# Kernel optimization log

Measured on AMD Instinct MI355X. Metric: run time of the kernel, lower is better.

## Reference

```python
import jax, jax.numpy as jnp
import numpy as np

V, BLOCK, D, H, L = 32000, 2048, 768, 12, 4
B, T = 2, 2048
HD = D // H
FF = 4 * D


def setup_inputs() -> dict:
    key = jax.random.key(0)
    ks = jax.random.split(key, 20)
    s = 0.02
    inp = {
        "idx": jax.random.randint(ks[0], (B, T), 0, V),
        "tok_emb": jax.random.normal(ks[1], (V, D), jnp.float32) * s,
        "pos_emb": jax.random.normal(ks[2], (BLOCK, D), jnp.float32) * s,
        # per-layer stacked params (leading dim L); linear weights stored [in, out]
        "ln1_w": jnp.ones((L, D), jnp.float32),
        "ln1_b": jnp.zeros((L, D), jnp.float32),
        "Wqkv": jax.random.normal(ks[3], (L, D, 3 * D), jnp.float32) * s,
        "bqkv": jnp.zeros((L, 3 * D), jnp.float32),
        "Wproj": jax.random.normal(ks[4], (L, D, D), jnp.float32) * s,
        "bproj": jnp.zeros((L, D), jnp.float32),
        "ln2_w": jnp.ones((L, D), jnp.float32),
        "ln2_b": jnp.zeros((L, D), jnp.float32),
        "Wfc": jax.random.normal(ks[5], (L, D, FF), jnp.float32) * s,
        "bfc": jnp.zeros((L, FF), jnp.float32),
        "Wfc2": jax.random.normal(ks[6], (L, FF, D), jnp.float32) * s,
        "bfc2": jnp.zeros((L, D), jnp.float32),
        "lnf_w": jnp.ones((D,), jnp.float32),
        "lnf_b": jnp.zeros((D,), jnp.float32),
    }
    return inp


def _layernorm(x, w, b, eps=1e-5):
    mu = jnp.mean(x, axis=-1, keepdims=True)
    var = jnp.var(x, axis=-1, keepdims=True)
    return (x - mu) * jax.lax.rsqrt(var + eps) * w + b


def _attn(x, Wqkv, bqkv, Wproj, bproj):
    b, t, c = x.shape
    qkv = x @ Wqkv + bqkv  # [B,T,3D]
    q, k, v = jnp.split(qkv, 3, axis=-1)
    q = q.reshape(b, t, H, HD)
    k = k.reshape(b, t, H, HD)
    v = v.reshape(b, t, H, HD)
    scale = 1.0 / np.sqrt(HD)
    att = jnp.einsum("bthd,bshd->bhts", q, k) * scale  # [B,H,T,T]
    causal = jnp.tril(jnp.ones((t, t), bool))
    att = jnp.where(causal[None, None], att, -jnp.inf)
    att = jax.nn.softmax(att, axis=-1)
    out = jnp.einsum("bhts,bshd->bthd", att, v).reshape(b, t, c)
    return out @ Wproj + bproj


def reference(idx, tok_emb, pos_emb, ln1_w, ln1_b, Wqkv, bqkv, Wproj, bproj,
              ln2_w, ln2_b, Wfc, bfc, Wfc2, bfc2, lnf_w, lnf_b):
    t = idx.shape[1]
    x = tok_emb[idx] + pos_emb[:t][None]  # [B,T,D]
    for l in range(L):
        h = _layernorm(x, ln1_w[l], ln1_b[l])
        x = x + _attn(h, Wqkv[l], bqkv[l], Wproj[l], bproj[l])
        h = _layernorm(x, ln2_w[l], ln2_b[l])
        h = jax.nn.gelu(h @ Wfc[l] + bfc[l], approximate=False) @ Wfc2[l] + bfc2[l]
        x = x + h
    x = _layernorm(x, lnf_w, lnf_b)
    return x @ tok_emb.T  # tied head, [B,T,V]
```

## Files before the change

kernel.cpp:

```cpp
#include <hip/hip_runtime.h>
#include <math.h>

#define VOCAB  32000
#define DMODEL 768
#define NHEAD  12
#define NLAYER 4
#define BATCH  2
#define SEQ    2048
#define HEADD  64
#define FFDIM  3072
#define MROWS  (BATCH*SEQ)

typedef __attribute__((ext_vector_type(8))) short bf16x8;
typedef __attribute__((ext_vector_type(4))) float f32x4;

__device__ __forceinline__ unsigned short f2bf(float f) {
    union { float f; unsigned u; } v; v.f = f;
    unsigned r = v.u + 0x7fffu + ((v.u >> 16) & 1u);
    return (unsigned short)(r >> 16);
}

__device__ __forceinline__ void async_lds16(const unsigned short* g, unsigned short* l) {
    __builtin_amdgcn_global_load_lds(
        (const __attribute__((address_space(1))) unsigned int*)(const void*)g,
        (__attribute__((address_space(3))) unsigned int*)(void*)l, 16, 0, 0);
}

__global__ void cvt_bf16_x4(const float* __restrict__ in, unsigned short* __restrict__ out, int n4) {
    int i = blockIdx.x * blockDim.x + threadIdx.x;
    if (i >= n4) return;
    float4 v = ((const float4*)in)[i];
    uint2 o;
    o.x = (unsigned)f2bf(v.x) | ((unsigned)f2bf(v.y) << 16);
    o.y = (unsigned)f2bf(v.z) | ((unsigned)f2bf(v.w) << 16);
    ((uint2*)out)[i] = o;
}

__global__ void transpose_cvt(const float* __restrict__ W, unsigned short* __restrict__ Wt,
                              int Kdim, int Ndim) {
    __shared__ float tile[32][33];
    int l  = blockIdx.z;
    int k0 = blockIdx.x * 32;
    int n0 = blockIdx.y * 32;
    const float* Wl = W + (size_t)l * Kdim * Ndim;
    unsigned short* Wtl = Wt + (size_t)l * Kdim * Ndim;
    int c = threadIdx.x & 31, r = threadIdx.x >> 5;
#pragma unroll
    for (int i = 0; i < 4; i++)
        tile[r + i * 8][c] = Wl[(size_t)(k0 + r + i * 8) * Ndim + n0 + c];
    __syncthreads();
#pragma unroll
    for (int i = 0; i < 4; i++)
        Wtl[(size_t)(n0 + r + i * 8) * Kdim + k0 + c] = f2bf(tile[c][r + i * 8]);
}

__global__ void embed_kernel(const int* __restrict__ idx, const float* __restrict__ tok,
                             const float* __restrict__ pos, float* __restrict__ x) {
    int row = blockIdx.x;
    int t = row & (SEQ - 1);
    int tr = idx[row];
    const float4* ts = (const float4*)(tok + (size_t)tr * DMODEL);
    const float4* ps = (const float4*)(pos + (size_t)t * DMODEL);
    float4* xs = (float4*)(x + (size_t)row * DMODEL);
    int i = threadIdx.x;
    float4 a = ts[i], b = ps[i];
    xs[i] = make_float4(a.x + b.x, a.y + b.y, a.z + b.z, a.w + b.w);
}

__global__ void layernorm_kernel(const float* __restrict__ x, const float* __restrict__ w,
                                 const float* __restrict__ b, unsigned short* __restrict__ out) {
    int row = blockIdx.x;
    const float* xr = x + (size_t)row * DMODEL;
    int t = threadIdx.x;
    float v0 = xr[t], v1 = xr[t + 256], v2 = xr[t + 512];
    float s = v0 + v1 + v2;
    float ss = v0 * v0 + v1 * v1 + v2 * v2;
#pragma unroll
    for (int off = 32; off >= 1; off >>= 1) {
        s  += __shfl_xor(s, off);
        ss += __shfl_xor(ss, off);
    }
    __shared__ float red[8];
    int wave = t >> 6, lane = t & 63;
    if (lane == 0) { red[wave] = s; red[wave + 4] = ss; }
    __syncthreads();
    s  = red[0] + red[1] + red[2] + red[3];
    ss = red[4] + red[5] + red[6] + red[7];
    float mu = s * (1.0f / DMODEL);
    float var = ss * (1.0f / DMODEL) - mu * mu;
    float rs = rsqrtf(var + 1e-5f);
    unsigned short* orow = out + (size_t)row * DMODEL;
    orow[t]       = f2bf((v0 - mu) * rs * w[t]       + b[t]);
    orow[t + 256] = f2bf((v1 - mu) * rs * w[t + 256] + b[t + 256]);
    orow[t + 512] = f2bf((v2 - mu) * rs * w[t + 512] + b[t + 512]);
}

template <bool GELU_, bool RESID_, bool OUTBF16_, bool BIAS_>
__global__ __launch_bounds__(256) void gemm_kernel(
    const unsigned short* __restrict__ A,
    const unsigned short* __restrict__ Bw,
    const float* __restrict__ bias,
    const float* resid,
    float* Cf, unsigned short* Cb,
    int Ndim, int Kdim) {
    const int bm = blockIdx.x * 128;
    const int bn = blockIdx.y * 128;
    __shared__ unsigned short As[128][32];
    __shared__ unsigned short Bs[128][32];
    int tid = threadIdx.x;
    int wave = tid >> 6, lane = tid & 63;
    int wm = (wave >> 1) * 64, wn = (wave & 1) * 64;
    int quad = lane >> 4, ln = lane & 15;
    int srow = lane >> 2;
    int scol = (lane & 3) * 8;
    f32x4 acc[4][4] = {};

    for (int k0 = 0; k0 < Kdim; k0 += 32) {
        __syncthreads();
#pragma unroll
        for (int i = 0; i < 2; i++) {
            int ch = (wave << 1) | i;
            async_lds16(A  + (size_t)(bm + ch * 16 + srow) * Kdim + k0 + scol, &As[ch * 16][0]);
            async_lds16(Bw + (size_t)(bn + ch * 16 + srow) * Kdim + k0 + scol, &Bs[ch * 16][0]);
        }
        __syncthreads();
        bf16x8 af[4], bfr[4];
#pragma unroll
        for (int tm = 0; tm < 4; tm++) af[tm]  = *(const bf16x8*)(&As[wm + tm * 16 + ln][quad * 8]);
#pragma unroll
        for (int tn = 0; tn < 4; tn++) bfr[tn] = *(const bf16x8*)(&Bs[wn + tn * 16 + ln][quad * 8]);
#pragma unroll
        for (int tm = 0; tm < 4; tm++)
#pragma unroll
            for (int tn = 0; tn < 4; tn++)
                acc[tm][tn] = __builtin_amdgcn_mfma_f32_16x16x32_bf16(af[tm], bfr[tn], acc[tm][tn], 0, 0, 0);
    }

#pragma unroll
    for (int tm = 0; tm < 4; tm++)
#pragma unroll
        for (int tn = 0; tn < 4; tn++)
#pragma unroll
            for (int r = 0; r < 4; r++) {
                int row = bm + wm + tm * 16 + quad * 4 + r;
                int col = bn + wn + tn * 16 + ln;
                float c = acc[tm][tn][r];
                if (BIAS_) c += bias[col];
                if (GELU_) c = 0.5f * c * (1.0f + erff(c * 0.70710678118654752f));
                if (RESID_) c += resid[(size_t)row * Ndim + col];
                if (OUTBF16_) Cb[(size_t)row * Ndim + col] = f2bf(c);
                else          Cf[(size_t)row * Ndim + col] = c;
            }
}

__global__ __launch_bounds__(256) void attn_kernel(const unsigned short* __restrict__ qkv,
                                                   unsigned short* __restrict__ out) {
    int qtile = blockIdx.x;
    int bh = blockIdx.y;
    int b = bh / NHEAD, h = bh % NHEAD;
    int q0 = qtile * 128;
    const unsigned short* base = qkv + (size_t)b * SEQ * (3 * DMODEL);

    __shared__ unsigned short Qs[128][72];
    __shared__ unsigned short Ks[64][72];
    __shared__ unsigned short Vs[64][72];
    __shared__ unsigned short Ps[128][72];

    int tid = threadIdx.x, wave = tid >> 6, lane = tid & 63;
    int quad = lane >> 4, ln = lane & 15;

    for (int c = tid; c < 1024; c += 256) {
        int r = c >> 3, col = (c & 7) * 8;
        *(bf16x8*)(&Qs[r][col]) =
            *(const bf16x8*)(base + (size_t)(q0 + r) * (3 * DMODEL) + h * HEADD + col);
    }
    __syncthreads();

    bf16x8 qf[2][2];
#pragma unroll
    for (int tm = 0; tm < 2; tm++)
#pragma unroll
        for (int ks = 0; ks < 2; ks++)
            qf[tm][ks] = *(const bf16x8*)(&Qs[wave * 32 + tm * 16 + ln][ks * 32 + quad * 8]);

    f32x4 o[2][4] = {};
    float mst[8], lst[8];
#pragma unroll
    for (int i = 0; i < 8; i++) { mst[i] = -3.0e38f; lst[i] = 0.0f; }

    const float scale = 0.125f;
    int nkt = qtile * 2 + 2;

    for (int kt = 0; kt < nkt; kt++) {
        __syncthreads();
        for (int c = tid; c < 512; c += 256) {
            int r = c >> 3, col = (c & 7) * 8;
            *(bf16x8*)(&Ks[r][col]) =
                *(const bf16x8*)(base + (size_t)(kt * 64 + r) * (3 * DMODEL) + DMODEL + h * HEADD + col);
            union { bf16x8 v; unsigned short u[8]; } vv;
            vv.v = *(const bf16x8*)(base + (size_t)(kt * 64 + r) * (3 * DMODEL) + 2 * DMODEL + h * HEADD + col);
#pragma unroll
            for (int j = 0; j < 8; j++) Vs[col + j][r] = vv.u[j];
        }
        __syncthreads();

        f32x4 s[2][4];
#pragma unroll
        for (int tm = 0; tm < 2; tm++)
#pragma unroll
            for (int tn = 0; tn < 4; tn++) s[tm][tn] = (f32x4){0.f, 0.f, 0.f, 0.f};
        bf16x8 kf[4][2];
#pragma unroll
        for (int tn = 0; tn < 4; tn++)
#pragma unroll
            for (int ks = 0; ks < 2; ks++)
                kf[tn][ks] = *(const bf16x8*)(&Ks[tn * 16 + ln][ks * 32 + quad * 8]);
#pragma unroll
        for (int tm = 0; tm < 2; tm++)
#pragma unroll
            for (int tn = 0; tn < 4; tn++)
#pragma unroll
                for (int ks = 0; ks < 2; ks++)
                    s[tm][tn] = __builtin_amdgcn_mfma_f32_16x16x32_bf16(qf[tm][ks], kf[tn][ks], s[tm][tn], 0, 0, 0);

#pragma unroll
        for (int tm = 0; tm < 2; tm++)
#pragma unroll
            for (int tn = 0; tn < 4; tn++)
#pragma unroll
                for (int r = 0; r < 4; r++) {
                    int qi = q0 + wave * 32 + tm * 16 + quad * 4 + r;
                    int kj = kt * 64 + tn * 16 + ln;
                    float sv = s[tm][tn][r] * scale;
                    s[tm][tn][r] = (kj > qi) ? -3.0e38f : sv;
                }

#pragma unroll
        for (int tm = 0; tm < 2; tm++)
#pragma unroll
            for (int r = 0; r < 4; r++) {
                float mx = fmaxf(fmaxf(s[tm][0][r], s[tm][1][r]), fmaxf(s[tm][2][r], s[tm][3][r]));
#pragma unroll
                for (int msk = 1; msk <= 8; msk <<= 1) mx = fmaxf(mx, __shfl_xor(mx, msk));
                int ri = tm * 4 + r;
                float mnew = fmaxf(mst[ri], mx);
                float alpha = __expf(mst[ri] - mnew);
                mst[ri] = mnew;
                float psum = 0.f;
#pragma unroll
                for (int tn = 0; tn < 4; tn++) {
                    float p = __expf(s[tm][tn][r] - mnew);
                    s[tm][tn][r] = p;
                    psum += p;
                }
#pragma unroll
                for (int msk = 1; msk <= 8; msk <<= 1) psum += __shfl_xor(psum, msk);
                lst[ri] = lst[ri] * alpha + psum;
#pragma unroll
                for (int nd = 0; nd < 4; nd++) o[tm][nd][r] *= alpha;
            }

#pragma unroll
        for (int tm = 0; tm < 2; tm++)
#pragma unroll
            for (int tn = 0; tn < 4; tn++)
#pragma unroll
                for (int r = 0; r < 4; r++)
                    Ps[wave * 32 + tm * 16 + quad * 4 + r][tn * 16 + ln] = f2bf(s[tm][tn][r]);

        bf16x8 pf[2][2], vf[4][2];
#pragma unroll
        for (int tm = 0; tm < 2; tm++)
#pragma unroll
            for (int ks = 0; ks < 2; ks++)
                pf[tm][ks] = *(const bf16x8*)(&Ps[wave * 32 + tm * 16 + ln][ks * 32 + quad * 8]);
#pragma unroll
        for (int nd = 0; nd < 4; nd++)
#pragma unroll
            for (int ks = 0; ks < 2; ks++)
                vf[nd][ks] = *(const bf16x8*)(&Vs[nd * 16 + ln][ks * 32 + quad * 8]);
#pragma unroll
        for (int tm = 0; tm < 2; tm++)
#pragma unroll
            for (int nd = 0; nd < 4; nd++)
#pragma unroll
                for (int ks = 0; ks < 2; ks++)
                    o[tm][nd] = __builtin_amdgcn_mfma_f32_16x16x32_bf16(pf[tm][ks], vf[nd][ks], o[tm][nd], 0, 0, 0);
    }

#pragma unroll
    for (int tm = 0; tm < 2; tm++)
#pragma unroll
        for (int r = 0; r < 4; r++) {
            float inv = 1.0f / lst[tm * 4 + r];
            int trow = q0 + wave * 32 + tm * 16 + quad * 4 + r;
#pragma unroll
            for (int nd = 0; nd < 4; nd++) {
                int col = h * HEADD + nd * 16 + ln;
                out[(size_t)(b * SEQ + trow) * DMODEL + col] = f2bf(o[tm][nd][r] * inv);
            }
        }
}

extern "C" void kernel_launch(void* const* d_in, const int* in_sizes, int n_in,
                              void* d_out, int out_size, void* d_ws, size_t ws_size,
                              hipStream_t stream) {
    const int*   idx   = (const int*)  d_in[0];
    const float* tok   = (const float*)d_in[1];
    const float* pos   = (const float*)d_in[2];
    const float* ln1w  = (const float*)d_in[3];
    const float* ln1b  = (const float*)d_in[4];
    const float* Wqkv  = (const float*)d_in[5];
    const float* bqkv  = (const float*)d_in[6];
    const float* Wproj = (const float*)d_in[7];
    const float* bproj = (const float*)d_in[8];
    const float* ln2w  = (const float*)d_in[9];
    const float* ln2b  = (const float*)d_in[10];
    const float* Wfc   = (const float*)d_in[11];
    const float* bfc   = (const float*)d_in[12];
    const float* Wfc2  = (const float*)d_in[13];
    const float* bfc2  = (const float*)d_in[14];
    const float* lnfw  = (const float*)d_in[15];
    const float* lnfb  = (const float*)d_in[16];

    char* ob = (char*)d_out;
    unsigned short* qkvb   = (unsigned short*)(ob + 0);
    float*          x      = (float*)(ob + 18874368);
    unsigned short* ffact  = (unsigned short*)(ob + 31457280);
    unsigned short* attnb  = (unsigned short*)(ob + 56623104);
    unsigned short* WqkvT  = (unsigned short*)(ob + 62914560);
    unsigned short* WprojT = (unsigned short*)(ob + 77070336);
    unsigned short* WfcT   = (unsigned short*)(ob + 81788928);
    unsigned short* Wfc2T  = (unsigned short*)(ob + 100663296);
    unsigned short* tokT   = (unsigned short*)d_ws;
    unsigned short* lnout  = (unsigned short*)((char*)d_ws + 49152000);

    cvt_bf16_x4<<<24000, 256, 0, stream>>>(tok, tokT, VOCAB * DMODEL / 4);
    transpose_cvt<<<dim3(24, 72, NLAYER), 256, 0, stream>>>(Wqkv,  WqkvT,  DMODEL, 3 * DMODEL);
    transpose_cvt<<<dim3(24, 24, NLAYER), 256, 0, stream>>>(Wproj, WprojT, DMODEL, DMODEL);
    transpose_cvt<<<dim3(24, 96, NLAYER), 256, 0, stream>>>(Wfc,   WfcT,   DMODEL, FFDIM);
    transpose_cvt<<<dim3(96, 24, NLAYER), 256, 0, stream>>>(Wfc2,  Wfc2T,  FFDIM,  DMODEL);

    embed_kernel<<<MROWS, 192, 0, stream>>>(idx, tok, pos, x);

    for (int l = 0; l < NLAYER; l++) {
        layernorm_kernel<<<MROWS, 256, 0, stream>>>(x, ln1w + l * DMODEL, ln1b + l * DMODEL, lnout);
        gemm_kernel<false, false, true, true><<<dim3(32, 18), 256, 0, stream>>>(
            lnout, WqkvT + (size_t)l * 3 * DMODEL * DMODEL, bqkv + l * 3 * DMODEL,
            nullptr, nullptr, qkvb, 3 * DMODEL, DMODEL);
        attn_kernel<<<dim3(16, BATCH * NHEAD), 256, 0, stream>>>(qkvb, attnb);
        gemm_kernel<false, true, false, true><<<dim3(32, 6), 256, 0, stream>>>(
            attnb, WprojT + (size_t)l * DMODEL * DMODEL, bproj + l * DMODEL,
            x, x, nullptr, DMODEL, DMODEL);
        layernorm_kernel<<<MROWS, 256, 0, stream>>>(x, ln2w + l * DMODEL, ln2b + l * DMODEL, lnout);
        gemm_kernel<true, false, true, true><<<dim3(32, 24), 256, 0, stream>>>(
            lnout, WfcT + (size_t)l * FFDIM * DMODEL, bfc + l * FFDIM,
            nullptr, nullptr, ffact, FFDIM, DMODEL);
        gemm_kernel<false, true, false, true><<<dim3(32, 6), 256, 0, stream>>>(
            ffact, Wfc2T + (size_t)l * FFDIM * DMODEL, bfc2 + l * DMODEL,
            x, x, nullptr, DMODEL, FFDIM);
    }

    layernorm_kernel<<<MROWS, 256, 0, stream>>>(x, lnfw, lnfb, lnout);
    gemm_kernel<false, false, false, false><<<dim3(32, 250), 256, 0, stream>>>(
        lnout, tokT, nullptr, nullptr, (float*)d_out, nullptr, VOCAB, DMODEL);
}
```

Before: 2.267 ms.

## Add 256x256 pipelined GEMM kernel for the tied LM head

Replaces the generic 128-tile GEMM for the final vocab projection with a new 512-thread kernel using 256x256 tiles, double-buffered LDS with XOR swizzle, and a four-phase schedule that interleaves async global-to-LDS loads with MFMA work using explicit vmcnt waits and s_setprio. The larger tile raises arithmetic intensity per loaded byte, and the phased staging is meant to hide memory latency behind MFMAs. It relies on hand-tuned waitcnt counts, so any miscount could race. It also uses much more LDS and registers per block, which may limit occupancy.

```diff
diff --git a/kernel.cpp b/kernel.cpp
--- a/kernel.cpp
+++ b/kernel.cpp
@@ -150,6 +150,116 @@
                 if (RESID_) c += resid[(size_t)row * Ndim + col];
                 if (OUTBF16_) Cb[(size_t)row * Ndim + col] = f2bf(c);
                 else          Cf[(size_t)row * Ndim + col] = c;
+            }
+}
+
+__device__ __forceinline__ void stage_Ax(const unsigned short* A, int Kdim, int bm,
+                                         unsigned short (*slotA)[64], int half, int ktile,
+                                         int w, int lrow, int scol) {
+#pragma unroll
+    for (int j = 0; j < 2; j++) {
+        int row = j * 128 + half * 64 + w * 8;
+        const unsigned short* src = A + (size_t)(bm + row + lrow) * Kdim + ktile * 64 + scol;
+        async_lds16(src, &slotA[row][0]);
+    }
+}
+__device__ __forceinline__ void stage_Bx(const unsigned short* Bw, int Kdim, int bn,
+                                         unsigned short (*slotB)[64], int half, int ktile,
+                                         int w, int lrow, int scol) {
+#pragma unroll
+    for (int j = 0; j < 2; j++) {
+        int gb = j * 64 + w * 8;
+        int row = (gb >> 5) * 64 + half * 32 + (gb & 31);
+        const unsigned short* src = Bw + (size_t)(bn + row + lrow) * Kdim + ktile * 64 + scol;
+        async_lds16(src, &slotB[row][0]);
+    }
+}
+
+#define PHASE(QM, QN, STAGE_STMT, VM_STMT)                                            \
+  { bf16x8 af[4][2], bfv[2][2];                                                        \
+    const char* Ab = (const char*)&lds[s][0][0][0];                                    \
+    const char* Bb = (const char*)&lds[s][1][0][0];                                    \
+    _Pragma("unroll") for (int j = 0; j < 4; j++) {                                    \
+      int row = wr * 128 + (QM) * 64 + j * 16 + ln;                                    \
+      int rs = row * 128, sw = (row & 7) << 4;                                         \
+      _Pragma("unroll") for (int ks = 0; ks < 2; ks++)                                 \
+        af[j][ks] = *(const bf16x8*)(Ab + rs + ((ks * 64 + quad * 16) ^ sw));          \
+    }                                                                                  \
+    _Pragma("unroll") for (int jn = 0; jn < 2; jn++) {                                 \
+      int row = wc * 64 + (QN) * 32 + jn * 16 + ln;                                    \
+      int rs = row * 128, sw = (row & 7) << 4;                                         \
+      _Pragma("unroll") for (int ks = 0; ks < 2; ks++)                                 \
+        bfv[jn][ks] = *(const bf16x8*)(Bb + rs + ((ks * 64 + quad * 16) ^ sw));        \
+    }                                                                                  \
+    STAGE_STMT;                                                                        \
+    VM_STMT;                                                                           \
+    __builtin_amdgcn_s_barrier(); asm volatile("" ::: "memory");                       \
+    asm volatile("s_waitcnt lgkmcnt(0)" ::: "memory");                                 \
+    __builtin_amdgcn_s_setprio(1);                                                     \
+    _Pragma("unroll") for (int j = 0; j < 4; j++)                                      \
+    _Pragma("unroll") for (int jn = 0; jn < 2; jn++)                                   \
+    _Pragma("unroll") for (int ks = 0; ks < 2; ks++)                                   \
+      acc[(QM) * 4 + j][(QN) * 2 + jn] = __builtin_amdgcn_mfma_f32_16x16x32_bf16(      \
+          af[j][ks], bfv[jn][ks], acc[(QM) * 4 + j][(QN) * 2 + jn], 0, 0, 0);          \
+    __builtin_amdgcn_s_setprio(0);                                                     \
+    __builtin_amdgcn_s_barrier(); asm volatile("" ::: "memory"); }
+
+__global__ __launch_bounds__(512, 2) void gemm256_kernel(
+    const unsigned short* __restrict__ A,
+    const unsigned short* __restrict__ Bw,
+    float* __restrict__ Cf, int Ndim, int Kdim) {
+    const int bm = blockIdx.x * 256;
+    const int bn = blockIdx.y * 256;
+    __shared__ unsigned short lds[2][2][256][64];
+    int tid = threadIdx.x;
+    int w = tid >> 6, lane = tid & 63;
+    int wr = w >> 2, wc = w & 3;
+    int quad = lane >> 4, ln = lane & 15;
+    int lrow = lane >> 3;
+    int scol = ((lane & 7) ^ lrow) << 3;
+    f32x4 acc[8][4] = {};
+    const int NT = Kdim >> 6;
+
+    stage_Ax(A,  Kdim, bm, lds[0][0], 0, 0, w, lrow, scol);
+    stage_Bx(Bw, Kdim, bn, lds[0][1], 0, 0, w, lrow, scol);
+    stage_Ax(A,  Kdim, bm, lds[0][0], 1, 0, w, lrow, scol);
+    stage_Bx(Bw, Kdim, bn, lds[0][1], 1, 0, w, lrow, scol);
+    stage_Ax(A,  Kdim, bm, lds[1][0], 0, 1, w, lrow, scol);
+    stage_Bx(Bw, Kdim, bn, lds[1][1], 0, 1, w, lrow, scol);
+    asm volatile("s_waitcnt vmcnt(8)" ::: "memory");
+    __builtin_amdgcn_s_barrier(); asm volatile("" ::: "memory");
+
+    for (int t = 0; t < NT; t++) {
+        const int s = t & 1;
+        unsigned short (*nA)[64] = lds[s ^ 1][0];
+        unsigned short (*nB)[64] = lds[s ^ 1][1];
+        unsigned short (*cA)[64] = lds[s][0];
+        unsigned short (*cB)[64] = lds[s][1];
+        const bool st1 = (t + 1 < NT), st2 = (t + 2 < NT);
+
+        PHASE(0, 0,
+              if (st1) stage_Ax(A, Kdim, bm, nA, 1, t + 1, w, lrow, scol),
+              if (st1) asm volatile("s_waitcnt vmcnt(6)" ::: "memory"))
+        PHASE(0, 1,
+              if (st1) stage_Bx(Bw, Kdim, bn, nB, 1, t + 1, w, lrow, scol),
+              if (st1) asm volatile("s_waitcnt vmcnt(10)" ::: "memory"))
+        PHASE(1, 0,
+              if (st2) stage_Ax(A, Kdim, bm, cA, 0, t + 2, w, lrow, scol), )
+        PHASE(1, 1,
+              if (st2) stage_Bx(Bw, Kdim, bn, cB, 0, t + 2, w, lrow, scol),
+              if (st2) { asm volatile("s_waitcnt vmcnt(8)" ::: "memory"); }
+              else if (t == NT - 2) { asm volatile("s_waitcnt vmcnt(0)" ::: "memory"); })
+    }
+
+#pragma unroll
+    for (int mf = 0; mf < 8; mf++)
+#pragma unroll
+        for (int nf = 0; nf < 4; nf++)
+#pragma unroll
+            for (int r = 0; r < 4; r++) {
+                int row = bm + wr * 128 + mf * 16 + quad * 4 + r;
+                int col = bn + wc * 64 + nf * 16 + ln;
+                Cf[(size_t)row * Ndim + col] = acc[mf][nf][r];
             }
 }
 
@@ -362,6 +472,5 @@
     }
 
     layernorm_kernel<<<MROWS, 256, 0, stream>>>(x, lnfw, lnfb, lnout);
-    gemm_kernel<false, false, false, false><<<dim3(32, 250), 256, 0, stream>>>(
-        lnout, tokT, nullptr, nullptr, (float*)d_out, nullptr, VOCAB, DMODEL);
-}
+    gemm256_kernel<<<dim3(16, 125), 512, 0, stream>>>(lnout, tokT, (float*)d_out, VOCAB, DMODEL);
+}
```

Result: no change. 2.244 ms (-1.0%).
